# Kernel tuning notes

Hardware: AMD Instinct MI355X
Metric: run time of the kernel (lower is better)

The kernel has to match this reference:

```python
import jax, jax.numpy as jnp
import numpy as np

B, N, IN_DIM, OUT_DIM, H = 8, 1024, 256, 256, 4
HD = OUT_DIM // H  # head_dim = 64
NEG = -1e9
EPS = 1e-5


def setup_inputs() -> dict:
    key = jax.random.key(0)
    ks = jax.random.split(key, 9)
    h = jax.random.normal(ks[0], (B, N, IN_DIM), dtype=jnp.float32)
    adj = jax.random.randint(ks[1], (N, N), 0, 2, dtype=jnp.int32)
    adj = adj.at[jnp.arange(N), jnp.arange(N)].set(1)  # self loops so no empty rows
    s = 1.0 / np.sqrt(IN_DIM)
    W = jax.random.uniform(ks[2], (H, IN_DIM, HD), jnp.float32, -s, s)
    sa = 1.0 / np.sqrt(2 * HD)
    a1 = jax.random.uniform(ks[3], (H, HD), jnp.float32, -sa, sa)
    a2 = jax.random.uniform(ks[4], (H, HD), jnp.float32, -sa, sa)
    sp = 1.0 / np.sqrt(OUT_DIM)
    proj_w = jax.random.uniform(ks[5], (OUT_DIM, OUT_DIM), jnp.float32, -sp, sp)
    proj_b = jax.random.uniform(ks[6], (OUT_DIM,), jnp.float32, -sp, sp)
    gamma = jnp.ones((OUT_DIM,), jnp.float32)
    beta = jnp.zeros((OUT_DIM,), jnp.float32)
    return {"h": h, "adj": adj, "W": W, "a1": a1, "a2": a2,
            "proj_w": proj_w, "proj_b": proj_b, "gamma": gamma, "beta": beta}


def reference(h, adj, W, a1, a2, proj_w, proj_b, gamma, beta):
    # Wh: [B,H,N,HD]
    Wh = jnp.einsum('bni,hid->bhnd', h, W)
    # Decompose a([Wh_i || Wh_j]) = a1.Wh_i + a2.Wh_j (same math as concat+linear)
    si = jnp.einsum('bhnd,hd->bhn', Wh, a1)  # [B,H,N]
    sj = jnp.einsum('bhnd,hd->bhn', Wh, a2)
    e = jax.nn.leaky_relu(si[:, :, :, None] + sj[:, :, None, :], 0.2)  # [B,H,N,N]
    mask = (adj == 0)  # [N,N]
    e = jnp.where(mask[None, None], NEG, e)
    alpha = jax.nn.softmax(e, axis=-1)
    out = jnp.einsum('bhnm,bhmd->bhnd', alpha, Wh)  # [B,H,N,HD]
    h_multi = out.transpose(0, 2, 1, 3).reshape(B, N, OUT_DIM)  # concat heads
    h_out = jnp.einsum('bnd,od->bno', h_multi, proj_w) + proj_b
    h_out = h_out + h  # residual (in_dim == out_dim)
    mu = jnp.mean(h_out, axis=-1, keepdims=True)
    var = jnp.mean(jnp.square(h_out - mu), axis=-1, keepdims=True)
    return (h_out - mu) * jax.lax.rsqrt(var + EPS) * gamma + beta
```

## Files before the change

### kernel.cpp

```cpp
#include <hip/hip_runtime.h>
#include <hip/hip_bf16.h>

#define NN 1024
#define LOG2E 1.44269504088896f

typedef __attribute__((ext_vector_type(8))) short short8;
typedef __attribute__((ext_vector_type(4))) float floatx4;
typedef __attribute__((ext_vector_type(4))) int intx4;
typedef __attribute__((ext_vector_type(2))) int intx2;

#define WAIT_VM0()   asm volatile("s_waitcnt vmcnt(0)" ::: "memory")
#define WAIT_LGKM0() asm volatile("s_waitcnt lgkmcnt(0)" ::: "memory")

static __device__ __forceinline__ unsigned pk2(float f0, float f1) {
    unsigned u0 = __float_as_uint(f0) + 0x8000u;
    unsigned u1 = __float_as_uint(f1) + 0x8000u;
    return __builtin_amdgcn_perm(u1, u0, 0x07060302u);
}
static __device__ __forceinline__ short8 pk8(floatx4 v0, floatx4 v1) {
    union { intx4 i; short8 s; } u;
    u.i[0] = (int)pk2(v0[0], v0[1]); u.i[1] = (int)pk2(v0[2], v0[3]);
    u.i[2] = (int)pk2(v1[0], v1[1]); u.i[3] = (int)pk2(v1[2], v1[3]);
    return u.s;
}
static __device__ __forceinline__ void load_lds16(const void* gsrc, void* lds) {
    __builtin_amdgcn_global_load_lds(
        (const __attribute__((address_space(1))) void*)gsrc,
        (__attribute__((address_space(3))) void*)lds, 16, 0, 0);
}

__global__ __launch_bounds__(256) void prep_kernel(
    const float* __restrict__ W, const float* __restrict__ proj_w,
    const int* __restrict__ adj,
    __hip_bfloat16* __restrict__ WTb,
    __hip_bfloat16* __restrict__ pwb,
    unsigned* __restrict__ adjm)
{
    int blk = blockIdx.x, t = threadIdx.x;
    if (blk < 16) {
        int o = blk * 16 + (t >> 4);
        int hh = o >> 6, d = o & 63;
        #pragma unroll
        for (int kk = 0; kk < 16; ++kk) {
            int k = (t & 15) + 16 * kk;
            WTb[(size_t)o * 256 + k] = __float2bfloat16(W[((size_t)hh * 256 + k) * 64 + d]);
        }
    } else if (blk < 32) {
        size_t base = (size_t)(blk - 16) * 4096 + (size_t)t * 16;
        #pragma unroll
        for (int k = 0; k < 16; k += 8) {
            floatx4 v0 = *(const floatx4*)(proj_w + base + k);
            floatx4 v1 = *(const floatx4*)(proj_w + base + k + 4);
            *(short8*)(pwb + base + k) = pk8(v0, v1);
        }
    } else {
        int n = (blk - 32) * 8 + (t >> 5);
        int wd = t & 31;
        const int* arow = adj + (size_t)n * NN + wd * 32;
        unsigned bits = 0;
        #pragma unroll
        for (int j4 = 0; j4 < 8; ++j4) {
            intx4 v = *(const intx4*)(arow + j4 * 4);
            #pragma unroll
            for (int j = 0; j < 4; ++j) if (v[j] != 0) bits |= (1u << (j4 * 4 + j));
        }
        adjm[(size_t)n * 32 + wd] = bits;
    }
}

__global__ __launch_bounds__(256) void wh_kernel(
    const float* __restrict__ h,
    const __hip_bfloat16* __restrict__ WTb,
    const float* __restrict__ a1, const float* __restrict__ a2,
    __hip_bfloat16* __restrict__ WhT,
    float* __restrict__ si, float* __restrict__ sj)
{
    int t = threadIdx.x;
    int w = t >> 6, l = t & 63;
    int rl = l & 15, q = l >> 4;
    int r0 = blockIdx.x * 16;
    int bb = r0 >> 10, n0 = r0 & 1023;

    __shared__ __align__(16) __hip_bfloat16 bst[4][4096];
    __shared__ float redsi[4][4][16];
    __shared__ float redsj[4][4][16];

    short8 af[8];
    const float* Arow = h + (size_t)(r0 + rl) * 256 + q * 8;
    #pragma unroll
    for (int k0 = 0; k0 < 8; ++k0) {
        floatx4 v0 = *(const floatx4*)(Arow + k0 * 32);
        floatx4 v1 = *(const floatx4*)(Arow + k0 * 32 + 4);
        af[k0] = pk8(v0, v1);
    }

    #pragma unroll
    for (int k = 0; k < 8; ++k) {
        int row = k * 2 + (l >> 5);
        int g = (l & 31) ^ (row & 7);
        load_lds16(WTb + (size_t)w * 4096 + row * 256 + g * 8, &bst[w][k * 512]);
    }

    #pragma unroll
    for (int j = 0; j < 4; ++j) {
        WAIT_VM0();
        floatx4 acc = {0.f, 0.f, 0.f, 0.f};
        #pragma unroll
        for (int k0 = 0; k0 < 8; ++k0) {
            int p = ((k0 << 2) + q) ^ (rl & 7);
            short8 bf = *(const short8*)(&bst[w][rl * 256 + p * 8]);
            acc = __builtin_amdgcn_mfma_f32_16x16x32_bf16(af[k0], bf, acc, 0, 0, 0);
        }
        WAIT_LGKM0();
        if (j < 3) {
            int ctn = w + 4 * (j + 1);
            #pragma unroll
            for (int k = 0; k < 8; ++k) {
                int row = k * 2 + (l >> 5);
                int g = (l & 31) ^ (row & 7);
                load_lds16(WTb + (size_t)ctn * 4096 + row * 256 + g * 8, &bst[w][k * 512]);
            }
        }

        intx2 pr;
        pr[0] = (int)pk2(acc[0], acc[1]);
        pr[1] = (int)pk2(acc[2], acc[3]);
        *(intx2*)(WhT + ((size_t)(bb * 4 + j) * 64 + w * 16 + rl) * NN + n0 + q * 4) = pr;

        float av1 = a1[j * 64 + w * 16 + rl] * LOG2E;
        float av2 = a2[j * 64 + w * 16 + rl] * LOG2E;
        #pragma unroll
        for (int i = 0; i < 4; ++i) {
            float p1 = acc[i] * av1, p2 = acc[i] * av2;
            #pragma unroll
            for (int off = 1; off < 16; off <<= 1) {
                p1 += __shfl_xor(p1, off, 64);
                p2 += __shfl_xor(p2, off, 64);
            }
            if (rl == 0) { redsi[w][j][q * 4 + i] = p1; redsj[w][j][q * 4 + i] = p2; }
        }
    }
    __syncthreads();

    if (t < 64) {
        int head = t >> 4, row = t & 15;
        si[(size_t)(bb * 4 + head) * NN + n0 + row] =
            redsi[0][head][row] + redsi[1][head][row] + redsi[2][head][row] + redsi[3][head][row];
    } else if (t < 128) {
        int u = t - 64;
        int head = u >> 4, row = u & 15;
        sj[(size_t)(bb * 4 + head) * NN + n0 + row] =
            redsj[0][head][row] + redsj[1][head][row] + redsj[2][head][row] + redsj[3][head][row];
    }
}

__global__ __launch_bounds__(256) void attn_proj_kernel(
    const unsigned* __restrict__ adjm,
    const __hip_bfloat16* __restrict__ WhT,
    const float* __restrict__ si, const float* __restrict__ sj,
    const __hip_bfloat16* __restrict__ pwb,
    const float* __restrict__ h,
    const float* __restrict__ proj_b, const float* __restrict__ gamma,
    const float* __restrict__ beta,
    float* __restrict__ out)
{
    __shared__ __align__(16) char smem[42752];
    auto bst   = reinterpret_cast<__hip_bfloat16 (*)[4096]>(smem);
    auto pl    = reinterpret_cast<__hip_bfloat16 (*)[16][72]>(smem + 32768);
    auto rinvs = reinterpret_cast<float (*)[16]>(smem + 41984);
    auto pbst  = reinterpret_cast<__hip_bfloat16 (*)[4096]>(smem);
    auto hm    = reinterpret_cast<__hip_bfloat16 (*)[264]>(smem + 32768);
    auto red   = reinterpret_cast<float (*)[4][16]>(smem + 42240);

    int bx = blockIdx.x, t = threadIdx.x;
    int w = t >> 6, l = t & 63;
    int rl = l & 15, q = l >> 4;
    int b = bx >> 6, n0 = (bx & 63) * 16;
    int bh = b * 4 + w;
    int r0 = bx * 16;

    int r = l >> 2, cg = l & 3;
    float sii = si[(size_t)bh * NN + n0 + r];
    const float* sjr = sj + (size_t)bh * NN;
    const unsigned* amrow = adjm + (size_t)(n0 + r) * 32;

    float lsum = 0.f;
    floatx4 acc[4] = { {0,0,0,0}, {0,0,0,0}, {0,0,0,0}, {0,0,0,0} };

    const __hip_bfloat16* Bhead = WhT + (size_t)bh * 64 * NN;
    int lrow = l >> 3;
    int lgrp = (l & 7) ^ lrow;

    for (int it = 0; it < 16; ++it) {
        int m0 = it * 64;
        #pragma unroll
        for (int k = 0; k < 8; ++k)
            load_lds16(Bhead + (size_t)(k * 8 + lrow) * NN + m0 + lgrp * 8, &bst[w][k * 512]);
        {
            int mb = m0 + cg * 16;
            unsigned bits = amrow[(m0 >> 5) + (cg >> 1)] >> ((cg & 1) * 16);
            #pragma unroll
            for (int c4 = 0; c4 < 4; ++c4) {
                floatx4 s4 = *(const floatx4*)(sjr + mb + c4 * 4);
                float pv[4];
                #pragma unroll
                for (int k = 0; k < 4; ++k) {
                    float x = sii + s4[k];
                    x = fmaxf(x, 0.2f * x);
                    x = ((bits >> (c4 * 4 + k)) & 1u) ? x : -1e9f;
                    pv[k] = exp2f(x);
                    lsum += pv[k];
                }
                intx2 two;
                two[0] = (int)pk2(pv[0], pv[1]);
                two[1] = (int)pk2(pv[2], pv[3]);
                *(intx2*)(&pl[w][r][cg * 16 + c4 * 4]) = two;
            }
        }
        WAIT_VM0();
        #pragma unroll
        for (int ks = 0; ks < 2; ++ks) {
            short8 afr = *(const short8*)(&pl[w][rl][ks * 32 + q * 8]);
            #pragma unroll
            for (int dt = 0; dt < 4; ++dt) {
                int p = ((ks << 2) + q) ^ (rl & 7);
                short8 bfr = *(const short8*)(&bst[w][(dt * 16 + rl) * 64 + p * 8]);
                acc[dt] = __builtin_amdgcn_mfma_f32_16x16x32_bf16(afr, bfr, acc[dt], 0, 0, 0);
            }
        }
        WAIT_LGKM0();
    }

    lsum += __shfl_xor(lsum, 1, 64);
    lsum += __shfl_xor(lsum, 2, 64);
    if (cg == 0) rinvs[w][r] = 1.f / lsum;
    float riv[4];
    #pragma unroll
    for (int i = 0; i < 4; ++i) riv[i] = rinvs[w][q * 4 + i];

    #pragma unroll
    for (int k = 0; k < 8; ++k) {
        int row = k * 2 + (l >> 5);
        int g = (l & 31) ^ (row & 7);
        load_lds16(pwb + (size_t)w * 4096 + row * 256 + g * 8, &pbst[w][k * 512]);
    }

    __syncthreads();
    #pragma unroll
    for (int dt = 0; dt < 4; ++dt) {
        #pragma unroll
        for (int i = 0; i < 4; ++i) {
            unsigned uv = (__float_as_uint(acc[dt][i] * riv[i]) + 0x8000u) >> 16;
            hm[q * 4 + i][w * 64 + dt * 16 + rl] = __ushort_as_bfloat16((unsigned short)uv);
        }
    }
    __syncthreads();

    short8 paf[8];
    #pragma unroll
    for (int k0 = 0; k0 < 8; ++k0) paf[k0] = *(const short8*)(&hm[rl][q * 8 + k0 * 32]);

    floatx4 pacc[4];
    #pragma unroll
    for (int j = 0; j < 4; ++j) {
        WAIT_VM0();
        floatx4 a = {0.f, 0.f, 0.f, 0.f};
        #pragma unroll
        for (int k0 = 0; k0 < 8; ++k0) {
            int p = ((k0 << 2) + q) ^ (rl & 7);
            short8 bf = *(const short8*)(&pbst[w][rl * 256 + p * 8]);
            a = __builtin_amdgcn_mfma_f32_16x16x32_bf16(paf[k0], bf, a, 0, 0, 0);
        }
        pacc[j] = a;
        WAIT_LGKM0();
        if (j < 3) {
            int ctn = w + 4 * (j + 1);
            #pragma unroll
            for (int k = 0; k < 8; ++k) {
                int row = k * 2 + (l >> 5);
                int g = (l & 31) ^ (row & 7);
                load_lds16(pwb + (size_t)ctn * 4096 + row * 256 + g * 8, &pbst[w][k * 512]);
            }
        }
    }

    float ps[4] = {0.f, 0.f, 0.f, 0.f};
    #pragma unroll
    for (int j = 0; j < 4; ++j) {
        int col = (w + j * 4) * 16 + rl;
        float pb = proj_b[col];
        #pragma unroll
        for (int i = 0; i < 4; ++i) {
            float v = pacc[j][i] + pb + h[(size_t)(r0 + q * 4 + i) * 256 + col];
            pacc[j][i] = v;
            ps[i] += v;
        }
    }
    #pragma unroll
    for (int i = 0; i < 4; ++i) {
        float s = ps[i];
        #pragma unroll
        for (int off = 1; off < 16; off <<= 1) s += __shfl_xor(s, off, 64);
        ps[i] = s;
    }
    if (rl == 0) {
        for (int i = 0; i < 4; ++i) red[0][w][q * 4 + i] = ps[i];
    }
    __syncthreads();
    float mu[4];
    #pragma unroll
    for (int i = 0; i < 4; ++i) {
        int row = q * 4 + i;
        mu[i] = (red[0][0][row] + red[0][1][row] + red[0][2][row] + red[0][3][row]) * (1.f / 256.f);
    }
    float vs[4] = {0.f, 0.f, 0.f, 0.f};
    #pragma unroll
    for (int j = 0; j < 4; ++j) {
        #pragma unroll
        for (int i = 0; i < 4; ++i) { float cv = pacc[j][i] - mu[i]; vs[i] += cv * cv; }
    }
    #pragma unroll
    for (int i = 0; i < 4; ++i) {
        float s = vs[i];
        #pragma unroll
        for (int off = 1; off < 16; off <<= 1) s += __shfl_xor(s, off, 64);
        vs[i] = s;
    }
    if (rl == 0) {
        for (int i = 0; i < 4; ++i) red[1][w][q * 4 + i] = vs[i];
    }
    __syncthreads();
    float rs[4];
    #pragma unroll
    for (int i = 0; i < 4; ++i) {
        int row = q * 4 + i;
        float var = (red[1][0][row] + red[1][1][row] + red[1][2][row] + red[1][3][row]) * (1.f / 256.f);
        rs[i] = rsqrtf(var + 1e-5f);
    }
    #pragma unroll
    for (int j = 0; j < 4; ++j) {
        int col = (w + j * 4) * 16 + rl;
        float g = gamma[col], be = beta[col];
        #pragma unroll
        for (int i = 0; i < 4; ++i)
            out[(size_t)(r0 + q * 4 + i) * 256 + col] = (pacc[j][i] - mu[i]) * rs[i] * g + be;
    }
}

extern "C" void kernel_launch(void* const* d_in, const int* in_sizes, int n_in,
                              void* d_out, int out_size, void* d_ws, size_t ws_size,
                              hipStream_t stream) {
    const float* h      = (const float*)d_in[0];
    const int*   adj    = (const int*)d_in[1];
    const float* W      = (const float*)d_in[2];
    const float* a1     = (const float*)d_in[3];
    const float* a2     = (const float*)d_in[4];
    const float* proj_w = (const float*)d_in[5];
    const float* proj_b = (const float*)d_in[6];
    const float* gamma  = (const float*)d_in[7];
    const float* beta   = (const float*)d_in[8];
    float* out = (float*)d_out;

    char* ws = (char*)d_ws;
    __hip_bfloat16* WhT = (__hip_bfloat16*)ws;   ws += (size_t)32 * 64 * NN * 2;
    __hip_bfloat16* WTb = (__hip_bfloat16*)ws;   ws += 256 * 256 * 2;
    __hip_bfloat16* pwb = (__hip_bfloat16*)ws;   ws += 256 * 256 * 2;
    float* si = (float*)ws;                      ws += (size_t)32 * NN * 4;
    float* sj = (float*)ws;                      ws += (size_t)32 * NN * 4;
    unsigned* adjm = (unsigned*)ws;              ws += (size_t)NN * 32 * 4;

    prep_kernel<<<160, 256, 0, stream>>>(W, proj_w, adj, WTb, pwb, adjm);
    wh_kernel<<<512, 256, 0, stream>>>(h, WTb, a1, a2, WhT, si, sj);
    attn_proj_kernel<<<512, 256, 0, stream>>>(adjm, WhT, si, sj, pwb, h, proj_b, gamma, beta, out);
}
```

Measured before the change: 120.5 us.

## Load MFMA B operands directly from global into registers instead of via LDS

```diff
diff --git a/kernel.cpp b/kernel.cpp
--- a/kernel.cpp
+++ b/kernel.cpp
@@ -8,9 +8,6 @@
 typedef __attribute__((ext_vector_type(4))) float floatx4;
 typedef __attribute__((ext_vector_type(4))) int intx4;
 typedef __attribute__((ext_vector_type(2))) int intx2;
-
-#define WAIT_VM0()   asm volatile("s_waitcnt vmcnt(0)" ::: "memory")
-#define WAIT_LGKM0() asm volatile("s_waitcnt lgkmcnt(0)" ::: "memory")
 
 static __device__ __forceinline__ unsigned pk2(float f0, float f1) {
     unsigned u0 = __float_as_uint(f0) + 0x8000u;
@@ -22,11 +19,6 @@
     u.i[0] = (int)pk2(v0[0], v0[1]); u.i[1] = (int)pk2(v0[2], v0[3]);
     u.i[2] = (int)pk2(v1[0], v1[1]); u.i[3] = (int)pk2(v1[2], v1[3]);
     return u.s;
-}
-static __device__ __forceinline__ void load_lds16(const void* gsrc, void* lds) {
-    __builtin_amdgcn_global_load_lds(
-        (const __attribute__((address_space(1))) void*)gsrc,
-        (__attribute__((address_space(3))) void*)lds, 16, 0, 0);
 }
 
 __global__ __launch_bounds__(256) void prep_kernel(
@@ -81,7 +73,6 @@
     int r0 = blockIdx.x * 16;
     int bb = r0 >> 10, n0 = r0 & 1023;
 
-    __shared__ __align__(16) __hip_bfloat16 bst[4][4096];
     __shared__ float redsi[4][4][16];
     __shared__ float redsj[4][4][16];
 
@@ -95,31 +86,14 @@
     }
 
     #pragma unroll
-    for (int k = 0; k < 8; ++k) {
-        int row = k * 2 + (l >> 5);
-        int g = (l & 31) ^ (row & 7);
-        load_lds16(WTb + (size_t)w * 4096 + row * 256 + g * 8, &bst[w][k * 512]);
-    }
-
-    #pragma unroll
-    for (int j = 0; j < 4; ++j) {
-        WAIT_VM0();
+    for (int j = 0; j < 4; ++j) {
+        int ct = w + 4 * j;
+        const __hip_bfloat16* Bp = WTb + (size_t)(ct * 16 + rl) * 256 + q * 8;
         floatx4 acc = {0.f, 0.f, 0.f, 0.f};
         #pragma unroll
         for (int k0 = 0; k0 < 8; ++k0) {
-            int p = ((k0 << 2) + q) ^ (rl & 7);
-            short8 bf = *(const short8*)(&bst[w][rl * 256 + p * 8]);
+            short8 bf = *(const short8*)(Bp + k0 * 32);
             acc = __builtin_amdgcn_mfma_f32_16x16x32_bf16(af[k0], bf, acc, 0, 0, 0);
-        }
-        WAIT_LGKM0();
-        if (j < 3) {
-            int ctn = w + 4 * (j + 1);
-            #pragma unroll
-            for (int k = 0; k < 8; ++k) {
-                int row = k * 2 + (l >> 5);
-                int g = (l & 31) ^ (row & 7);
-                load_lds16(WTb + (size_t)ctn * 4096 + row * 256 + g * 8, &bst[w][k * 512]);
-            }
         }
 
         intx2 pr;
@@ -164,13 +138,10 @@
     const float* __restrict__ beta,
     float* __restrict__ out)
 {
-    __shared__ __align__(16) char smem[42752];
-    auto bst   = reinterpret_cast<__hip_bfloat16 (*)[4096]>(smem);
-    auto pl    = reinterpret_cast<__hip_bfloat16 (*)[16][72]>(smem + 32768);
-    auto rinvs = reinterpret_cast<float (*)[16]>(smem + 41984);
-    auto pbst  = reinterpret_cast<__hip_bfloat16 (*)[4096]>(smem);
-    auto hm    = reinterpret_cast<__hip_bfloat16 (*)[264]>(smem + 32768);
-    auto red   = reinterpret_cast<float (*)[4][16]>(smem + 42240);
+    __shared__ __align__(16) __hip_bfloat16 pl[4][16][72];
+    __shared__ float rinvs[4][16];
+    __shared__ __align__(16) __hip_bfloat16 hm[16][264];
+    __shared__ float red[2][4][16];
 
     int bx = blockIdx.x, t = threadIdx.x;
     int w = t >> 6, l = t & 63;
@@ -188,14 +159,25 @@
     floatx4 acc[4] = { {0,0,0,0}, {0,0,0,0}, {0,0,0,0}, {0,0,0,0} };
 
     const __hip_bfloat16* Bhead = WhT + (size_t)bh * 64 * NN;
-    int lrow = l >> 3;
-    int lgrp = (l & 7) ^ lrow;
-
+
+    short8 bf[8];
+    #pragma unroll
+    for (int u = 0; u < 8; ++u) {
+        int ks = u >> 2, dt = u & 3;
+        bf[u] = *(const short8*)(Bhead + (size_t)(dt * 16 + rl) * NN + ks * 32 + q * 8);
+    }
+
+    #pragma unroll 2
     for (int it = 0; it < 16; ++it) {
         int m0 = it * 64;
-        #pragma unroll
-        for (int k = 0; k < 8; ++k)
-            load_lds16(Bhead + (size_t)(k * 8 + lrow) * NN + m0 + lgrp * 8, &bst[w][k * 512]);
+        short8 bn[8];
+        if (it < 15) {
+            #pragma unroll
+            for (int u = 0; u < 8; ++u) {
+                int ks = u >> 2, dt = u & 3;
+                bn[u] = *(const short8*)(Bhead + (size_t)(dt * 16 + rl) * NN + m0 + 64 + ks * 32 + q * 8);
+            }
+        }
         {
             int mb = m0 + cg * 16;
             unsigned bits = amrow[(m0 >> 5) + (cg >> 1)] >> ((cg & 1) * 16);
@@ -217,18 +199,17 @@
                 *(intx2*)(&pl[w][r][cg * 16 + c4 * 4]) = two;
             }
         }
-        WAIT_VM0();
         #pragma unroll
         for (int ks = 0; ks < 2; ++ks) {
             short8 afr = *(const short8*)(&pl[w][rl][ks * 32 + q * 8]);
             #pragma unroll
-            for (int dt = 0; dt < 4; ++dt) {
-                int p = ((ks << 2) + q) ^ (rl & 7);
-                short8 bfr = *(const short8*)(&bst[w][(dt * 16 + rl) * 64 + p * 8]);
-                acc[dt] = __builtin_amdgcn_mfma_f32_16x16x32_bf16(afr, bfr, acc[dt], 0, 0, 0);
-            }
-        }
-        WAIT_LGKM0();
+            for (int dt = 0; dt < 4; ++dt)
+                acc[dt] = __builtin_amdgcn_mfma_f32_16x16x32_bf16(afr, bf[ks * 4 + dt], acc[dt], 0, 0, 0);
+        }
+        if (it < 15) {
+            #pragma unroll
+            for (int u = 0; u < 8; ++u) bf[u] = bn[u];
+        }
     }
 
     lsum += __shfl_xor(lsum, 1, 64);
@@ -239,14 +220,6 @@
     for (int i = 0; i < 4; ++i) riv[i] = rinvs[w][q * 4 + i];
 
     #pragma unroll
-    for (int k = 0; k < 8; ++k) {
-        int row = k * 2 + (l >> 5);
-        int g = (l & 31) ^ (row & 7);
-        load_lds16(pwb + (size_t)w * 4096 + row * 256 + g * 8, &pbst[w][k * 512]);
-    }
-
-    __syncthreads();
-    #pragma unroll
     for (int dt = 0; dt < 4; ++dt) {
         #pragma unroll
         for (int i = 0; i < 4; ++i) {
@@ -263,25 +236,15 @@
     floatx4 pacc[4];
     #pragma unroll
     for (int j = 0; j < 4; ++j) {
-        WAIT_VM0();
+        int ct = w + 4 * j;
+        const __hip_bfloat16* Bp = pwb + (size_t)(ct * 16 + rl) * 256 + q * 8;
         floatx4 a = {0.f, 0.f, 0.f, 0.f};
         #pragma unroll
         for (int k0 = 0; k0 < 8; ++k0) {
-            int p = ((k0 << 2) + q) ^ (rl & 7);
-            short8 bf = *(const short8*)(&pbst[w][rl * 256 + p * 8]);
-            a = __builtin_amdgcn_mfma_f32_16x16x32_bf16(paf[k0], bf, a, 0, 0, 0);
+            short8 bfp = *(const short8*)(Bp + k0 * 32);
+            a = __builtin_amdgcn_mfma_f32_16x16x32_bf16(paf[k0], bfp, a, 0, 0, 0);
         }
         pacc[j] = a;
-        WAIT_LGKM0();
-        if (j < 3) {
-            int ctn = w + 4 * (j + 1);
-            #pragma unroll
-            for (int k = 0; k < 8; ++k) {
-                int row = k * 2 + (l >> 5);
-                int g = (l & 31) ^ (row & 7);
-                load_lds16(pwb + (size_t)ctn * 4096 + row * 256 + g * 8, &pbst[w][k * 512]);
-            }
-        }
     }
 
     float ps[4] = {0.f, 0.f, 0.f, 0.f};
```

New measurement: 140.5 us. +16.6%, slower.

## Split attention key range across two wave groups with 512-thread blocks

Applied to the files above, without the earlier changes.

```diff
diff --git a/kernel.cpp b/kernel.cpp
--- a/kernel.cpp
+++ b/kernel.cpp
@@ -154,7 +154,7 @@
     }
 }
 
-__global__ __launch_bounds__(256) void attn_proj_kernel(
+__global__ __launch_bounds__(512, 4) void attn_proj_kernel(
     const unsigned* __restrict__ adjm,
     const __hip_bfloat16* __restrict__ WhT,
     const float* __restrict__ si, const float* __restrict__ sj,
@@ -164,19 +164,19 @@
     const float* __restrict__ beta,
     float* __restrict__ out)
 {
-    __shared__ __align__(16) char smem[42752];
-    auto bst   = reinterpret_cast<__hip_bfloat16 (*)[4096]>(smem);
-    auto pl    = reinterpret_cast<__hip_bfloat16 (*)[16][72]>(smem + 32768);
-    auto rinvs = reinterpret_cast<float (*)[16]>(smem + 41984);
-    auto pbst  = reinterpret_cast<__hip_bfloat16 (*)[4096]>(smem);
-    auto hm    = reinterpret_cast<__hip_bfloat16 (*)[264]>(smem + 32768);
-    auto red   = reinterpret_cast<float (*)[4][16]>(smem + 42240);
+    __shared__ __align__(16) __hip_bfloat16 bst[8][2048];
+    __shared__ __align__(16) __hip_bfloat16 pl[8][16][40];
+    __shared__ float lsums[2][4][16];
+    __shared__ __align__(16) __hip_bfloat16 hm[16][264];
+    __shared__ float red[2][8][16];
+    float (*accx)[64][20] = reinterpret_cast<float (*)[64][20]>(&bst[0][0]);
 
     int bx = blockIdx.x, t = threadIdx.x;
     int w = t >> 6, l = t & 63;
+    int hh = w & 3, e = w >> 2;
     int rl = l & 15, q = l >> 4;
     int b = bx >> 6, n0 = (bx & 63) * 16;
-    int bh = b * 4 + w;
+    int bh = b * 4 + hh;
     int r0 = bx * 16;
 
     int r = l >> 2, cg = l & 3;
@@ -188,19 +188,21 @@
     floatx4 acc[4] = { {0,0,0,0}, {0,0,0,0}, {0,0,0,0}, {0,0,0,0} };
 
     const __hip_bfloat16* Bhead = WhT + (size_t)bh * 64 * NN;
-    int lrow = l >> 3;
-    int lgrp = (l & 7) ^ lrow;
+
+    int srow = l >> 2;
+    int sg = (l & 3) ^ (srow & 3);
+
+    #pragma unroll
+    for (int k = 0; k < 4; ++k)
+        load_lds16(Bhead + (size_t)(k * 16 + srow) * NN + e * 32 + sg * 8, &bst[w][k * 512]);
 
     for (int it = 0; it < 16; ++it) {
-        int m0 = it * 64;
-        #pragma unroll
-        for (int k = 0; k < 8; ++k)
-            load_lds16(Bhead + (size_t)(k * 8 + lrow) * NN + m0 + lgrp * 8, &bst[w][k * 512]);
+        int mw = it * 64 + e * 32;
         {
-            int mb = m0 + cg * 16;
-            unsigned bits = amrow[(m0 >> 5) + (cg >> 1)] >> ((cg & 1) * 16);
-            #pragma unroll
-            for (int c4 = 0; c4 < 4; ++c4) {
+            unsigned bits = amrow[it * 2 + e] >> (cg * 8);
+            int mb = mw + cg * 8;
+            #pragma unroll
+            for (int c4 = 0; c4 < 2; ++c4) {
                 floatx4 s4 = *(const floatx4*)(sjr + mb + c4 * 4);
                 float pv[4];
                 #pragma unroll
@@ -214,44 +216,54 @@
                 intx2 two;
                 two[0] = (int)pk2(pv[0], pv[1]);
                 two[1] = (int)pk2(pv[2], pv[3]);
-                *(intx2*)(&pl[w][r][cg * 16 + c4 * 4]) = two;
+                *(intx2*)(&pl[w][r][cg * 8 + c4 * 4]) = two;
             }
         }
         WAIT_VM0();
-        #pragma unroll
-        for (int ks = 0; ks < 2; ++ks) {
-            short8 afr = *(const short8*)(&pl[w][rl][ks * 32 + q * 8]);
-            #pragma unroll
-            for (int dt = 0; dt < 4; ++dt) {
-                int p = ((ks << 2) + q) ^ (rl & 7);
-                short8 bfr = *(const short8*)(&bst[w][(dt * 16 + rl) * 64 + p * 8]);
-                acc[dt] = __builtin_amdgcn_mfma_f32_16x16x32_bf16(afr, bfr, acc[dt], 0, 0, 0);
-            }
+        short8 afr = *(const short8*)(&pl[w][rl][q * 8]);
+        #pragma unroll
+        for (int dt = 0; dt < 4; ++dt) {
+            short8 bfr = *(const short8*)(&bst[w][(dt * 16 + rl) * 32 + (q ^ (rl & 3)) * 8]);
+            acc[dt] = __builtin_amdgcn_mfma_f32_16x16x32_bf16(afr, bfr, acc[dt], 0, 0, 0);
         }
         WAIT_LGKM0();
+        if (it < 15) {
+            int mwn = mw + 64;
+            #pragma unroll
+            for (int k = 0; k < 4; ++k)
+                load_lds16(Bhead + (size_t)(k * 16 + srow) * NN + mwn + sg * 8, &bst[w][k * 512]);
+        }
     }
 
     lsum += __shfl_xor(lsum, 1, 64);
     lsum += __shfl_xor(lsum, 2, 64);
-    if (cg == 0) rinvs[w][r] = 1.f / lsum;
-    float riv[4];
-    #pragma unroll
-    for (int i = 0; i < 4; ++i) riv[i] = rinvs[w][q * 4 + i];
-
-    #pragma unroll
-    for (int k = 0; k < 8; ++k) {
-        int row = k * 2 + (l >> 5);
-        int g = (l & 31) ^ (row & 7);
-        load_lds16(pwb + (size_t)w * 4096 + row * 256 + g * 8, &pbst[w][k * 512]);
-    }
-
-    __syncthreads();
-    #pragma unroll
-    for (int dt = 0; dt < 4; ++dt) {
-        #pragma unroll
-        for (int i = 0; i < 4; ++i) {
-            unsigned uv = (__float_as_uint(acc[dt][i] * riv[i]) + 0x8000u) >> 16;
-            hm[q * 4 + i][w * 64 + dt * 16 + rl] = __ushort_as_bfloat16((unsigned short)uv);
+    if (cg == 0) lsums[e][hh][r] = lsum;
+
+    __syncthreads();
+
+    if (e == 1) {
+        #pragma unroll
+        for (int dt = 0; dt < 4; ++dt) {
+            #pragma unroll
+            for (int i = 0; i < 4; ++i)
+                accx[hh][l][dt * 4 + i] = acc[dt][i];
+        }
+    }
+    __syncthreads();
+
+    if (e == 0) {
+        float riv[4];
+        #pragma unroll
+        for (int i = 0; i < 4; ++i)
+            riv[i] = 1.f / (lsums[0][hh][q * 4 + i] + lsums[1][hh][q * 4 + i]);
+        #pragma unroll
+        for (int dt = 0; dt < 4; ++dt) {
+            #pragma unroll
+            for (int i = 0; i < 4; ++i) {
+                float v = acc[dt][i] + accx[hh][l][dt * 4 + i];
+                unsigned uv = (__float_as_uint(v * riv[i]) + 0x8000u) >> 16;
+                hm[q * 4 + i][hh * 64 + dt * 16 + rl] = __ushort_as_bfloat16((unsigned short)uv);
+            }
         }
     }
     __syncthreads();
@@ -260,34 +272,24 @@
     #pragma unroll
     for (int k0 = 0; k0 < 8; ++k0) paf[k0] = *(const short8*)(&hm[rl][q * 8 + k0 * 32]);
 
-    floatx4 pacc[4];
-    #pragma unroll
-    for (int j = 0; j < 4; ++j) {
-        WAIT_VM0();
+    floatx4 pacc[2];
+    #pragma unroll
+    for (int j = 0; j < 2; ++j) {
+        int ct = w + 8 * j;
+        const __hip_bfloat16* Bp = pwb + (size_t)(ct * 16 + rl) * 256 + q * 8;
         floatx4 a = {0.f, 0.f, 0.f, 0.f};
         #pragma unroll
         for (int k0 = 0; k0 < 8; ++k0) {
-            int p = ((k0 << 2) + q) ^ (rl & 7);
-            short8 bf = *(const short8*)(&pbst[w][rl * 256 + p * 8]);
-            a = __builtin_amdgcn_mfma_f32_16x16x32_bf16(paf[k0], bf, a, 0, 0, 0);
+            short8 bfp = *(const short8*)(Bp + k0 * 32);
+            a = __builtin_amdgcn_mfma_f32_16x16x32_bf16(paf[k0], bfp, a, 0, 0, 0);
         }
         pacc[j] = a;
-        WAIT_LGKM0();
-        if (j < 3) {
-            int ctn = w + 4 * (j + 1);
-            #pragma unroll
-            for (int k = 0; k < 8; ++k) {
-                int row = k * 2 + (l >> 5);
-                int g = (l & 31) ^ (row & 7);
-                load_lds16(pwb + (size_t)ctn * 4096 + row * 256 + g * 8, &pbst[w][k * 512]);
-            }
-        }
     }
 
     float ps[4] = {0.f, 0.f, 0.f, 0.f};
     #pragma unroll
-    for (int j = 0; j < 4; ++j) {
-        int col = (w + j * 4) * 16 + rl;
+    for (int j = 0; j < 2; ++j) {
+        int col = (w + 8 * j) * 16 + rl;
         float pb = proj_b[col];
         #pragma unroll
         for (int i = 0; i < 4; ++i) {
@@ -311,11 +313,14 @@
     #pragma unroll
     for (int i = 0; i < 4; ++i) {
         int row = q * 4 + i;
-        mu[i] = (red[0][0][row] + red[0][1][row] + red[0][2][row] + red[0][3][row]) * (1.f / 256.f);
+        float s = 0.f;
+        #pragma unroll
+        for (int ww = 0; ww < 8; ++ww) s += red[0][ww][row];
+        mu[i] = s * (1.f / 256.f);
     }
     float vs[4] = {0.f, 0.f, 0.f, 0.f};
     #pragma unroll
-    for (int j = 0; j < 4; ++j) {
+    for (int j = 0; j < 2; ++j) {
         #pragma unroll
         for (int i = 0; i < 4; ++i) { float cv = pacc[j][i] - mu[i]; vs[i] += cv * cv; }
     }
@@ -334,12 +339,14 @@
     #pragma unroll
     for (int i = 0; i < 4; ++i) {
         int row = q * 4 + i;
-        float var = (red[1][0][row] + red[1][1][row] + red[1][2][row] + red[1][3][row]) * (1.f / 256.f);
-        rs[i] = rsqrtf(var + 1e-5f);
-    }
-    #pragma unroll
-    for (int j = 0; j < 4; ++j) {
-        int col = (w + j * 4) * 16 + rl;
+        float s = 0.f;
+        #pragma unroll
+        for (int ww = 0; ww < 8; ++ww) s += red[1][ww][row];
+        rs[i] = rsqrtf(s * (1.f / 256.f) + 1e-5f);
+    }
+    #pragma unroll
+    for (int j = 0; j < 2; ++j) {
+        int col = (w + 8 * j) * 16 + rl;
         float g = gamma[col], be = beta[col];
         #pragma unroll
         for (int i = 0; i < 4; ++i)
@@ -371,5 +378,5 @@
 
     prep_kernel<<<160, 256, 0, stream>>>(W, proj_w, adj, WTb, pwb, adjm);
     wh_kernel<<<512, 256, 0, stream>>>(h, WTb, a1, a2, WhT, si, sj);
-    attn_proj_kernel<<<512, 256, 0, stream>>>(adjm, WhT, si, sj, pwb, h, proj_b, gamma, beta, out);
-}
+    attn_proj_kernel<<<512, 512, 0, stream>>>(adjm, WhT, si, sj, pwb, h, proj_b, gamma, beta, out);
+}
```

Result: no change. 122.7 us (+1.8%).
